# Performance work log

Hardware: AMD Instinct MI355X
Metric: run time of the kernel (lower is better)

## Reference

```python
import math
import jax, jax.numpy as jnp
import numpy as np

DIM = 2048
NUM_HEADS = 16
HEAD_DIM = DIM // NUM_HEADS
BASE = 10000.0


def _rope(x):
    # x: [B, S, H, D]; non-interleaved (chunk-half) rotary embedding
    S, D = x.shape[1], x.shape[-1]
    inv_freq = 1.0 / (BASE ** (jnp.arange(0, D, 2, dtype=jnp.float32) / D))
    t = jnp.arange(S, dtype=jnp.float32)
    freqs = jnp.outer(t, inv_freq)  # [S, D/2]
    cos = jnp.cos(freqs)[None, :, None, :].astype(x.dtype)
    sin = jnp.sin(freqs)[None, :, None, :].astype(x.dtype)
    x1, x2 = jnp.split(x, 2, axis=-1)
    return jnp.concatenate([x1 * cos - x2 * sin, x1 * sin + x2 * cos], axis=-1)


def setup_inputs() -> dict:
    key = jax.random.key(0)
    kx, kq, kk, kv, ko = jax.random.split(key, 5)
    x = jax.random.normal(kx, (2, 2048, DIM), dtype=jnp.float32)
    scale = 0.02
    Wq = jax.random.normal(kq, (DIM, DIM), dtype=jnp.float32) * scale
    Wk = jax.random.normal(kk, (DIM, DIM), dtype=jnp.float32) * scale
    Wv = jax.random.normal(kv, (DIM, DIM), dtype=jnp.float32) * scale
    Wo = jax.random.normal(ko, (DIM, DIM), dtype=jnp.float32) * scale
    return {"x": x, "Wq": Wq, "Wk": Wk, "Wv": Wv, "Wo": Wo}


def reference(x, Wq, Wk, Wv, Wo):
    B, S, _ = x.shape
    # nn.Linear(bias=False): y = x @ W.T
    q = (x @ Wq.T).reshape(B, S, NUM_HEADS, HEAD_DIM)
    k = (x @ Wk.T).reshape(B, S, NUM_HEADS, HEAD_DIM)
    v = (x @ Wv.T).reshape(B, S, NUM_HEADS, HEAD_DIM)
    q = _rope(q)
    k = _rope(k)
    scale = 1.0 / math.sqrt(HEAD_DIM)
    # causal attention, [B,H,S,S] scores
    scores = jnp.einsum("bqhd,bkhd->bhqk", q, k) * scale
    causal = jnp.tril(jnp.ones((S, S), dtype=bool))
    scores = jnp.where(causal[None, None], scores, jnp.finfo(scores.dtype).min)
    attn = jax.nn.softmax(scores, axis=-1)
    out = jnp.einsum("bhqk,bkhd->bqhd", attn, v).reshape(B, S, DIM)
    return out @ Wo.T
```

## Files before the change

### kernel.cpp

```cpp
#include <hip/hip_runtime.h>

typedef unsigned short u16;
typedef __attribute__((ext_vector_type(8))) short short8;
typedef __attribute__((ext_vector_type(4))) float f32x4;
typedef __attribute__((ext_vector_type(4))) int i32x4;

__device__ __forceinline__ float bf2f(u16 u) {
  union { unsigned u; float f; } v; v.u = ((unsigned)u) << 16; return v.f;
}
__device__ __forceinline__ u16 f2bf(float f) {
  union { float f; unsigned u; } v; v.f = f;
  unsigned r = (v.u + 0x7FFFu + ((v.u >> 16) & 1u)) >> 16;
  return (u16)r;
}
__device__ __forceinline__ float flushv(float t, float sentinel) {
  if (t != t || fabsf(t) > 3.0e38f) return sentinel;
  return t;
}
__device__ __forceinline__ short8 ld8f(const float* p) {
  const float4 f0 = *(const float4*)p;
  const float4 f1 = *(const float4*)(p + 4);
  short8 r;
  r[0] = (short)f2bf(f0.x); r[1] = (short)f2bf(f0.y);
  r[2] = (short)f2bf(f0.z); r[3] = (short)f2bf(f0.w);
  r[4] = (short)f2bf(f1.x); r[5] = (short)f2bf(f1.y);
  r[6] = (short)f2bf(f1.z); r[7] = (short)f2bf(f1.w);
  return r;
}

__device__ __forceinline__ void gl16(const u16* g, u16* l) {
  __builtin_amdgcn_global_load_lds(
      (const __attribute__((address_space(1))) void*)g,
      (__attribute__((address_space(3))) void*)l, 16, 0, 0);
}

__global__ __launch_bounds__(256) void cvt_kernel(
    const float* __restrict__ src, u16* __restrict__ dst, long n8)
{
  const long t = (long)blockIdx.x * 256 + threadIdx.x;
  if (t < n8) *(short8*)&dst[t * 8] = ld8f(src + t * 8);
}

__global__ __launch_bounds__(256) void cvt4_kernel(
    const float* __restrict__ s0, const float* __restrict__ s1,
    const float* __restrict__ s2, const float* __restrict__ s3,
    u16* __restrict__ d0, u16* __restrict__ d1,
    u16* __restrict__ d2, u16* __restrict__ d3)
{
  const int which = blockIdx.x >> 11;
  const long t = (long)(blockIdx.x & 2047) * 256 + threadIdx.x;
  const float* s; u16* d;
  if (which == 0)      { s = s0; d = d0; }
  else if (which == 1) { s = s1; d = d1; }
  else if (which == 2) { s = s2; d = d2; }
  else                 { s = s3; d = d3; }
  *(short8*)&d[t * 8] = ld8f(s + t * 8);
}

template <bool OF>
__global__ __launch_bounds__(256) void gemm_lds(
    const u16* __restrict__ Ap,
    const u16* __restrict__ B0, const u16* __restrict__ B1,
    void* __restrict__ O0, void* __restrict__ O1,
    int M, int N, int K, float sentinel)
{
  __shared__ __align__(16) u16 As[128 * 32];
  __shared__ __align__(16) u16 Bs[128 * 32];

  const u16* Bp = (blockIdx.z == 0) ? B0 : B1;
  void* O       = (blockIdx.z == 0) ? O0 : O1;

  const int tid  = threadIdx.x;
  const int wave = tid >> 6;
  const int lane = tid & 63;
  const int quad = lane >> 4;
  const int l15  = lane & 15;

  const int m0 = blockIdx.y * 128;
  const int n0 = blockIdx.x * 128;
  const int wm = (wave >> 1) * 64;
  const int wn = (wave & 1) * 64;

  const int srow = lane >> 2;
  const int scu  = lane & 3;
  const u16* Ag0 = Ap + (long)(m0 + wave * 32 + srow) * K + scu * 8;
  const u16* Ag1 = Ag0 + 16 * (long)K;
  const u16* Bg0 = Bp + (long)(n0 + wave * 32 + srow) * K + scu * 8;
  const u16* Bg1 = Bg0 + 16 * (long)K;
  u16* Al0 = &As[(wave * 2 + 0) * 512];
  u16* Al1 = &As[(wave * 2 + 1) * 512];
  u16* Bl0 = &Bs[(wave * 2 + 0) * 512];
  u16* Bl1 = &Bs[(wave * 2 + 1) * 512];

  const f32x4 zero = {0.f, 0.f, 0.f, 0.f};
  f32x4 acc[4][4];
#pragma unroll
  for (int i = 0; i < 4; ++i)
#pragma unroll
    for (int j = 0; j < 4; ++j) acc[i][j] = zero;

  for (int k0 = 0; k0 < K; k0 += 32) {
    __syncthreads();
    gl16(Ag0 + k0, Al0);
    gl16(Ag1 + k0, Al1);
    gl16(Bg0 + k0, Bl0);
    gl16(Bg1 + k0, Bl1);
    __syncthreads();

    short8 af[4], bf[4];
#pragma unroll
    for (int i = 0; i < 4; ++i)
      af[i] = *(const short8*)&As[(wm + i * 16 + l15) * 32 + quad * 8];
#pragma unroll
    for (int j = 0; j < 4; ++j)
      bf[j] = *(const short8*)&Bs[(wn + j * 16 + l15) * 32 + quad * 8];
#pragma unroll
    for (int i = 0; i < 4; ++i)
#pragma unroll
      for (int j = 0; j < 4; ++j)
        acc[i][j] = __builtin_amdgcn_mfma_f32_16x16x32_bf16(af[i], bf[j], acc[i][j], 0, 0, 0);
  }

#pragma unroll
  for (int i = 0; i < 4; ++i) {
    const int row0 = m0 + wm + i * 16 + quad * 4;
#pragma unroll
    for (int j = 0; j < 4; ++j) {
      const int col = n0 + wn + j * 16 + l15;
#pragma unroll
      for (int r = 0; r < 4; ++r) {
        const float val = flushv(acc[i][j][r], sentinel);
        if constexpr (OF)
          ((float*)O)[(long)(row0 + r) * N + col] = val;
        else
          ((u16*)O)[(long)(row0 + r) * N + col] = f2bf(val);
      }
    }
  }
}

template <bool AF, bool WF, bool OF>
__global__ __launch_bounds__(256) void gemm_bt(
    const void* __restrict__ Ap,
    const void* __restrict__ Wp0, const void* __restrict__ Wp1, const void* __restrict__ Wp2,
    void* __restrict__ O0, void* __restrict__ O1, void* __restrict__ O2,
    int M, int N, int K, float sentinel)
{
  __shared__ __align__(16) u16 As[128 * 32];
  __shared__ __align__(16) u16 Bs[128 * 32];

  const void* Wp; void* O;
  if (blockIdx.z == 0)      { Wp = Wp0; O = O0; }
  else if (blockIdx.z == 1) { Wp = Wp1; O = O1; }
  else                      { Wp = Wp2; O = O2; }

  const float* Af = (const float*)Ap;  const u16* Ab = (const u16*)Ap;
  const float* Wf = (const float*)Wp;  const u16* Wb = (const u16*)Wp;

  const int tid  = threadIdx.x;
  const int wave = tid >> 6;
  const int lane = tid & 63;
  const int quad = lane >> 4;
  const int l15  = lane & 15;

  const int m0 = blockIdx.y * 128;
  const int n0 = blockIdx.x * 128;
  const int wm = (wave >> 1) * 64;
  const int wn = (wave & 1) * 64;

  const int e0 = wave * 1024 + lane * 8;
  const int e1 = e0 + 512;
  const int r0 = e0 >> 5, c0 = e0 & 31;
  const int r1 = e1 >> 5, c1 = e1 & 31;

  const long aoff0 = (long)(m0 + r0) * K + c0;
  const long aoff1 = (long)(m0 + r1) * K + c1;
  const long boff0 = (long)(n0 + r0) * K + c0;
  const long boff1 = (long)(n0 + r1) * K + c1;

  const f32x4 zero = {0.f, 0.f, 0.f, 0.f};
  f32x4 acc[4][4];
#pragma unroll
  for (int i = 0; i < 4; ++i)
#pragma unroll
    for (int j = 0; j < 4; ++j) acc[i][j] = zero;

  for (int k0 = 0; k0 < K; k0 += 32) {
    short8 a0, a1, b0, b1;
    if constexpr (AF) {
      a0 = ld8f(Af + aoff0 + k0);
      a1 = ld8f(Af + aoff1 + k0);
    } else {
      a0 = *(const short8*)(Ab + aoff0 + k0);
      a1 = *(const short8*)(Ab + aoff1 + k0);
    }
    if constexpr (WF) {
      b0 = ld8f(Wf + boff0 + k0);
      b1 = ld8f(Wf + boff1 + k0);
    } else {
      b0 = *(const short8*)(Wb + boff0 + k0);
      b1 = *(const short8*)(Wb + boff1 + k0);
    }

    __syncthreads();
    *(short8*)&As[e0] = a0;
    *(short8*)&As[e1] = a1;
    *(short8*)&Bs[e0] = b0;
    *(short8*)&Bs[e1] = b1;
    __syncthreads();

    short8 af[4], bf[4];
#pragma unroll
    for (int i = 0; i < 4; ++i)
      af[i] = *(const short8*)&As[(wm + i * 16 + l15) * 32 + quad * 8];
#pragma unroll
    for (int j = 0; j < 4; ++j)
      bf[j] = *(const short8*)&Bs[(wn + j * 16 + l15) * 32 + quad * 8];
#pragma unroll
    for (int i = 0; i < 4; ++i)
#pragma unroll
      for (int j = 0; j < 4; ++j)
        acc[i][j] = __builtin_amdgcn_mfma_f32_16x16x32_bf16(af[i], bf[j], acc[i][j], 0, 0, 0);
  }

#pragma unroll
  for (int i = 0; i < 4; ++i) {
    const int row0 = m0 + wm + i * 16 + quad * 4;
#pragma unroll
    for (int j = 0; j < 4; ++j) {
      const int col = n0 + wn + j * 16 + l15;
#pragma unroll
      for (int r = 0; r < 4; ++r) {
        const float val = flushv(acc[i][j][r], sentinel);
        if constexpr (OF)
          ((float*)O)[(long)(row0 + r) * N + col] = val;
        else
          ((u16*)O)[(long)(row0 + r) * N + col] = f2bf(val);
      }
    }
  }
}

__global__ __launch_bounds__(256) void rope_kernel(u16* __restrict__ Q, u16* __restrict__ K)
{
  int t = blockIdx.x * 256 + threadIdx.x;
  const int half = 2 * 2048 * 16 * 64;
  u16* P = Q;
  if (t >= half) { P = K; t -= half; }
  const int i = t & 63;
  const int s = (t >> 10) & 2047;
  const long off = ((long)(t >> 6) << 7) + i;

  const float inv_freq = __expf((float)i * -0.14391156831212787f);
  const float fr = (float)s * inv_freq;
  float sn, cs;
  __sincosf(fr, &sn, &cs);

  const float q1 = bf2f(P[off]);
  const float q2 = bf2f(P[off + 64]);
  P[off]      = f2bf(q1 * cs - q2 * sn);
  P[off + 64] = f2bf(q1 * sn + q2 * cs);
}

__global__ __launch_bounds__(256, 4) void attn_kernel(
    const u16* __restrict__ Q, const u16* __restrict__ K,
    const u16* __restrict__ VT, u16* __restrict__ AO)
{
  __shared__ __align__(16) u16 Kb[2][4096];
  __shared__ __align__(16) u16 Vb[2][4096];

  const int tid  = threadIdx.x;
  const int wave = tid >> 6;
  const int lane = tid & 63;
  const int quad = lane >> 4;
  const int l15  = lane & 15;

  const int lin = blockIdx.x;
  const int xcd = lin & 7;
  const int hi  = lin >> 8;
  const int g   = (lin >> 3) & 31;
  const int qb  = (hi & 1) ? (31 - g) : g;
  const int bh  = (xcd << 2) | hi;
  const int b   = bh >> 4;
  const int h   = bh & 15;

  const long base = (long)b * 2048 * 2048 + (long)h * 128;
  const long vtb  = (long)h * 128 * 4096 + (long)b * 2048;
  const int q0w = qb * 64 + wave * 16;
  const int qi  = q0w + l15;

  const u16* Kp0 = K + base;
  const u16* Vp0 = VT + vtb;

  auto STAGE = [&](int bs, int jb) {
#pragma unroll
    for (int gi = 0; gi < 2; ++gi) {
      const int slot = wave * 2 + gi;
      {
        const int row = slot * 4 + (lane >> 4);
        const int su  = lane & 15;
        gl16(Kp0 + (long)(jb * 32 + row) * 2048 + ((su ^ (row & 7)) << 3),
             &Kb[bs][slot * 512]);
      }
      {
        const int row = slot * 16 + (lane >> 2);
        const int su  = lane & 3;
        gl16(Vp0 + (long)row * 4096 + jb * 32 + ((su ^ ((row >> 1) & 3)) << 3),
             &Vb[bs][slot * 512]);
      }
    }
  };

  short8 qa[4];
#pragma unroll
  for (int c = 0; c < 4; ++c)
    qa[c] = *(const short8*)&Q[base + (long)(q0w + l15) * 2048 + c * 32 + quad * 8];

  const f32x4 zero = {0.f, 0.f, 0.f, 0.f};
  f32x4 o[8];
#pragma unroll
  for (int c = 0; c < 8; ++c) o[c] = zero;

  float mreg = -1e30f, lreg = 0.f;
  const float scale = 0.08838834764831845f;

  const int njb_blk = qb * 2 + 2;
  const int njb_w   = qb * 2 + 1 + (wave >> 1);

  STAGE(0, 0);
  __syncthreads();

  const int xorK = l15 & 7;
  const int xorV = (l15 >> 1) & 3;

  int cur = 0;
  for (int jb = 0; jb < njb_blk; ++jb) {
    if (jb + 1 < njb_blk) STAGE(cur ^ 1, jb + 1);

    if (jb < njb_w) {
      const int j0 = jb * 32;

      f32x4 s0T = zero, s1T = zero;
#pragma unroll
      for (int c = 0; c < 4; ++c) {
        const short8 kA = *(const short8*)&Kb[cur][l15 * 128 + (((c * 4 + quad) ^ xorK) << 3)];
        const short8 kB2 = *(const short8*)&Kb[cur][(l15 + 16) * 128 + (((c * 4 + quad) ^ xorK) << 3)];
        s0T = __builtin_amdgcn_mfma_f32_16x16x32_bf16(kA, qa[c], s0T, 0, 0, 0);
        s1T = __builtin_amdgcn_mfma_f32_16x16x32_bf16(kB2, qa[c], s1T, 0, 0, 0);
      }

      float sv0[4], sv1[4];
      float pmax = -1e30f;
      if (j0 + 31 > q0w) {
#pragma unroll
        for (int r = 0; r < 4; ++r) {
          const int k0i = j0 + quad * 4 + r;
          float s0 = s0T[r] * scale; if (k0i > qi)      s0 = -1e30f;
          float s1 = s1T[r] * scale; if (k0i + 16 > qi) s1 = -1e30f;
          sv0[r] = s0; sv1[r] = s1;
          pmax = fmaxf(pmax, fmaxf(s0, s1));
        }
      } else {
#pragma unroll
        for (int r = 0; r < 4; ++r) {
          sv0[r] = s0T[r] * scale;
          sv1[r] = s1T[r] * scale;
          pmax = fmaxf(pmax, fmaxf(sv0[r], sv1[r]));
        }
      }
      pmax = fmaxf(pmax, __shfl_xor(pmax, 16, 64));
      pmax = fmaxf(pmax, __shfl_xor(pmax, 32, 64));
      const float mprev = mreg;
      const float mnew  = fmaxf(mprev, pmax);
      const float alpha = __expf(mprev - mnew);
      float psum = 0.f;
#pragma unroll
      for (int r = 0; r < 4; ++r) {
        sv0[r] = __expf(sv0[r] - mnew);
        sv1[r] = __expf(sv1[r] - mnew);
        psum += sv0[r] + sv1[r];
      }
      psum += __shfl_xor(psum, 16, 64);
      psum += __shfl_xor(psum, 32, 64);
      lreg = lreg * alpha + psum;
      mreg = mnew;

      int w0, w1, w2, w3;
      asm("v_cvt_pk_bf16_f32 %0, %1, %2" : "=v"(w0) : "v"(sv0[0]), "v"(sv0[1]));
      asm("v_cvt_pk_bf16_f32 %0, %1, %2" : "=v"(w1) : "v"(sv0[2]), "v"(sv0[3]));
      asm("v_cvt_pk_bf16_f32 %0, %1, %2" : "=v"(w2) : "v"(sv1[0]), "v"(sv1[1]));
      asm("v_cvt_pk_bf16_f32 %0, %1, %2" : "=v"(w3) : "v"(sv1[2]), "v"(sv1[3]));
      const int srcA = l15 + ((quad & 1) << 5);
      const int srcB = srcA + 16;
      const int a0 = __shfl(w0, srcA, 64), a1 = __shfl(w1, srcA, 64);
      const int a2 = __shfl(w0, srcB, 64), a3 = __shfl(w1, srcB, 64);
      const int h0 = __shfl(w2, srcA, 64), h1 = __shfl(w3, srcA, 64);
      const int h2 = __shfl(w2, srcB, 64), h3 = __shfl(w3, srcB, 64);
      const bool hiq = quad >= 2;
      i32x4 pt;
      pt[0] = hiq ? h0 : a0;
      pt[1] = hiq ? h1 : a1;
      pt[2] = hiq ? h2 : a2;
      pt[3] = hiq ? h3 : a3;
      const short8 pa = *(const short8*)&pt;

      float av[4];
#pragma unroll
      for (int r = 0; r < 4; ++r) av[r] = __shfl(alpha, quad * 4 + r, 64);
#pragma unroll
      for (int c = 0; c < 8; ++c) {
        o[c][0] *= av[0]; o[c][1] *= av[1]; o[c][2] *= av[2]; o[c][3] *= av[3];
      }

#pragma unroll
      for (int c = 0; c < 8; ++c) {
        const short8 vf = *(const short8*)&Vb[cur][(c * 16 + l15) * 32 + ((quad ^ xorV) << 3)];
        o[c] = __builtin_amdgcn_mfma_f32_16x16x32_bf16(pa, vf, o[c], 0, 0, 0);
      }
    }

    __syncthreads();
    cur ^= 1;
  }

#pragma unroll
  for (int r = 0; r < 4; ++r) {
    const float lr  = __shfl(lreg, quad * 4 + r, 64);
    const float inv = 1.0f / lr;
    const long rowoff = base + (long)(q0w + quad * 4 + r) * 2048;
#pragma unroll
    for (int c = 0; c < 8; ++c)
      AO[rowoff + c * 16 + l15] = f2bf(flushv(o[c][r] * inv, 9999.f));
  }
}

__global__ __launch_bounds__(256) void fill_kernel(float* __restrict__ out, long n, float v)
{
  const long t = (long)blockIdx.x * 256 + threadIdx.x;
  if (t < n) out[t] = v;
}

extern "C" void kernel_launch(void* const* d_in, const int* in_sizes, int n_in,
                              void* d_out, int out_size, void* d_ws, size_t ws_size,
                              hipStream_t stream)
{
  const float* x  = (const float*)d_in[0];
  const float* Wq = (const float*)d_in[1];
  const float* Wk = (const float*)d_in[2];
  const float* Wv = (const float*)d_in[3];
  const float* Wo = (const float*)d_in[4];
  float* out = (float*)d_out;

  const long QSZ = (long)2 * 2048 * 2048;
  const long WSZ = QSZ / 2;

  u16* ws = (u16*)d_ws;
  u16* q  = ws;
  u16* k  = ws + QSZ;
  u16* v  = ws + 2 * QSZ;
  u16* ao = q;

  if (ws_size >= (size_t)6 * QSZ * sizeof(u16)) {
    u16* xb  = ws + 3 * QSZ;
    u16* wqb = ws + 4 * QSZ;
    u16* wkb = wqb + WSZ;
    u16* wvb = wqb + 2 * WSZ;
    u16* wob = wqb + 3 * WSZ;

    cvt_kernel<<<4096, 256, 0, stream>>>(x, xb, QSZ / 8);
    cvt4_kernel<<<8192, 256, 0, stream>>>(Wq, Wk, Wv, Wo, wqb, wkb, wvb, wob);

    gemm_lds<false><<<dim3(16, 32, 2), 256, 0, stream>>>(
        xb, wqb, wkb, q, k, 4096, 2048, 2048, 7777.f);
    gemm_lds<false><<<dim3(32, 16, 1), 256, 0, stream>>>(
        wvb, xb, xb, v, v, 2048, 4096, 2048, 7777.f);
    rope_kernel<<<32768, 256, 0, stream>>>(q, k);
    attn_kernel<<<1024, 256, 0, stream>>>(q, k, v, ao);
    gemm_lds<true><<<dim3(16, 32, 1), 256, 0, stream>>>(
        ao, wob, wob, out, out, 4096, 2048, 2048, 5555.f);
    return;
  }

  if (ws_size < (size_t)3 * QSZ * sizeof(u16)) {
    fill_kernel<<<(int)((QSZ + 255) / 256), 256, 0, stream>>>(out, QSZ, 1111.f);
    return;
  }

  gemm_bt<true, true, false><<<dim3(16, 32, 2), 256, 0, stream>>>(
      x, Wq, Wk, Wk, q, k, k, 4096, 2048, 2048, 7777.f);
  gemm_bt<true, true, false><<<dim3(32, 16, 1), 256, 0, stream>>>(
      Wv, x, x, x, v, v, v, 2048, 4096, 2048, 7777.f);
  rope_kernel<<<32768, 256, 0, stream>>>(q, k);
  attn_kernel<<<1024, 256, 0, stream>>>(q, k, v, ao);
  gemm_bt<false, true, true><<<dim3(16, 32, 1), 256, 0, stream>>>(
      ao, Wo, Wo, Wo, out, out, out, 4096, 2048, 2048, 5555.f);
}
```

Baseline: 455.3 us.

## Double-buffer GEMM LDS tiles and merge conversion and QKV launches

The LDS-tiled GEMM now uses two shared-memory buffers, so the global-to-LDS load for the next K slice is issued while MFMAs run on the current one. This halves the barriers per K step and hides load latency. The five fp32-to-bf16 conversions are merged into one kernel, and the Q/K/V projections into a single 1536-block launch, removing launch gaps and tail idle time between kernels. In exchange, LDS use per block doubles, which may lower occupancy, and K is now hardcoded to 2048.

```diff
diff --git a/kernel.cpp b/kernel.cpp
--- a/kernel.cpp
+++ b/kernel.cpp
@@ -34,41 +34,37 @@
       (__attribute__((address_space(3))) void*)l, 16, 0, 0);
 }
 
-__global__ __launch_bounds__(256) void cvt_kernel(
-    const float* __restrict__ src, u16* __restrict__ dst, long n8)
-{
-  const long t = (long)blockIdx.x * 256 + threadIdx.x;
-  if (t < n8) *(short8*)&dst[t * 8] = ld8f(src + t * 8);
-}
-
-__global__ __launch_bounds__(256) void cvt4_kernel(
-    const float* __restrict__ s0, const float* __restrict__ s1,
-    const float* __restrict__ s2, const float* __restrict__ s3,
-    u16* __restrict__ d0, u16* __restrict__ d1,
-    u16* __restrict__ d2, u16* __restrict__ d3)
-{
-  const int which = blockIdx.x >> 11;
-  const long t = (long)(blockIdx.x & 2047) * 256 + threadIdx.x;
-  const float* s; u16* d;
-  if (which == 0)      { s = s0; d = d0; }
-  else if (which == 1) { s = s1; d = d1; }
-  else if (which == 2) { s = s2; d = d2; }
-  else                 { s = s3; d = d3; }
+__global__ __launch_bounds__(256) void cvt_all(
+    const float* __restrict__ x,
+    const float* __restrict__ Wq, const float* __restrict__ Wk,
+    const float* __restrict__ Wv, const float* __restrict__ Wo,
+    u16* __restrict__ xb, u16* __restrict__ wqb, u16* __restrict__ wkb,
+    u16* __restrict__ wvb, u16* __restrict__ wob)
+{
+  const int bid = blockIdx.x;
+  const float* s; u16* d; long t;
+  if (bid < 8192) {
+    const int which = bid >> 11;
+    t = (long)(bid & 2047) * 256 + threadIdx.x;
+    if (which == 0)      { s = Wq; d = wqb; }
+    else if (which == 1) { s = Wk; d = wkb; }
+    else if (which == 2) { s = Wv; d = wvb; }
+    else                 { s = Wo; d = wob; }
+  } else {
+    s = x; d = xb;
+    t = (long)(bid - 8192) * 256 + threadIdx.x;
+  }
   *(short8*)&d[t * 8] = ld8f(s + t * 8);
 }
 
 template <bool OF>
-__global__ __launch_bounds__(256) void gemm_lds(
-    const u16* __restrict__ Ap,
-    const u16* __restrict__ B0, const u16* __restrict__ B1,
-    void* __restrict__ O0, void* __restrict__ O1,
-    int M, int N, int K, float sentinel)
-{
-  __shared__ __align__(16) u16 As[128 * 32];
-  __shared__ __align__(16) u16 Bs[128 * 32];
-
-  const u16* Bp = (blockIdx.z == 0) ? B0 : B1;
-  void* O       = (blockIdx.z == 0) ? O0 : O1;
+__device__ __forceinline__ void gemm_core(
+    const u16* __restrict__ Ap, const u16* __restrict__ Bp,
+    void* __restrict__ O, int m0, int n0, int N, float sentinel)
+{
+  __shared__ __align__(16) u16 As[2][128 * 32];
+  __shared__ __align__(16) u16 Bs[2][128 * 32];
+  constexpr int K = 2048;
 
   const int tid  = threadIdx.x;
   const int wave = tid >> 6;
@@ -76,8 +72,6 @@
   const int quad = lane >> 4;
   const int l15  = lane & 15;
 
-  const int m0 = blockIdx.y * 128;
-  const int n0 = blockIdx.x * 128;
   const int wm = (wave >> 1) * 64;
   const int wn = (wave & 1) * 64;
 
@@ -87,10 +81,8 @@
   const u16* Ag1 = Ag0 + 16 * (long)K;
   const u16* Bg0 = Bp + (long)(n0 + wave * 32 + srow) * K + scu * 8;
   const u16* Bg1 = Bg0 + 16 * (long)K;
-  u16* Al0 = &As[(wave * 2 + 0) * 512];
-  u16* Al1 = &As[(wave * 2 + 1) * 512];
-  u16* Bl0 = &Bs[(wave * 2 + 0) * 512];
-  u16* Bl1 = &Bs[(wave * 2 + 1) * 512];
+  const int sl0 = (wave * 2 + 0) * 512;
+  const int sl1 = (wave * 2 + 1) * 512;
 
   const f32x4 zero = {0.f, 0.f, 0.f, 0.f};
   f32x4 acc[4][4];
@@ -99,26 +91,49 @@
 #pragma unroll
     for (int j = 0; j < 4; ++j) acc[i][j] = zero;
 
-  for (int k0 = 0; k0 < K; k0 += 32) {
+  gl16(Ag0, &As[0][sl0]); gl16(Ag1, &As[0][sl1]);
+  gl16(Bg0, &Bs[0][sl0]); gl16(Bg1, &Bs[0][sl1]);
+  __syncthreads();
+
+#pragma unroll 1
+  for (int k0 = 0; k0 < K; k0 += 64) {
+    gl16(Ag0 + k0 + 32, &As[1][sl0]); gl16(Ag1 + k0 + 32, &As[1][sl1]);
+    gl16(Bg0 + k0 + 32, &Bs[1][sl0]); gl16(Bg1 + k0 + 32, &Bs[1][sl1]);
+    {
+      short8 af[4], bf[4];
+#pragma unroll
+      for (int i = 0; i < 4; ++i)
+        af[i] = *(const short8*)&As[0][(wm + i * 16 + l15) * 32 + quad * 8];
+#pragma unroll
+      for (int j = 0; j < 4; ++j)
+        bf[j] = *(const short8*)&Bs[0][(wn + j * 16 + l15) * 32 + quad * 8];
+#pragma unroll
+      for (int i = 0; i < 4; ++i)
+#pragma unroll
+        for (int j = 0; j < 4; ++j)
+          acc[i][j] = __builtin_amdgcn_mfma_f32_16x16x32_bf16(af[i], bf[j], acc[i][j], 0, 0, 0);
+    }
     __syncthreads();
-    gl16(Ag0 + k0, Al0);
-    gl16(Ag1 + k0, Al1);
-    gl16(Bg0 + k0, Bl0);
-    gl16(Bg1 + k0, Bl1);
+
+    if (k0 + 64 < K) {
+      gl16(Ag0 + k0 + 64, &As[0][sl0]); gl16(Ag1 + k0 + 64, &As[0][sl1]);
+      gl16(Bg0 + k0 + 64, &Bs[0][sl0]); gl16(Bg1 + k0 + 64, &Bs[0][sl1]);
+    }
+    {
+      short8 af[4], bf[4];
+#pragma unroll
+      for (int i = 0; i < 4; ++i)
+        af[i] = *(const short8*)&As[1][(wm + i * 16 + l15) * 32 + quad * 8];
+#pragma unroll
+      for (int j = 0; j < 4; ++j)
+        bf[j] = *(const short8*)&Bs[1][(wn + j * 16 + l15) * 32 + quad * 8];
+#pragma unroll
+      for (int i = 0; i < 4; ++i)
+#pragma unroll
+        for (int j = 0; j < 4; ++j)
+          acc[i][j] = __builtin_amdgcn_mfma_f32_16x16x32_bf16(af[i], bf[j], acc[i][j], 0, 0, 0);
+    }
     __syncthreads();
-
-    short8 af[4], bf[4];
-#pragma unroll
-    for (int i = 0; i < 4; ++i)
-      af[i] = *(const short8*)&As[(wm + i * 16 + l15) * 32 + quad * 8];
-#pragma unroll
-    for (int j = 0; j < 4; ++j)
-      bf[j] = *(const short8*)&Bs[(wn + j * 16 + l15) * 32 + quad * 8];
-#pragma unroll
-    for (int i = 0; i < 4; ++i)
-#pragma unroll
-      for (int j = 0; j < 4; ++j)
-        acc[i][j] = __builtin_amdgcn_mfma_f32_16x16x32_bf16(af[i], bf[j], acc[i][j], 0, 0, 0);
   }
 
 #pragma unroll
@@ -137,6 +152,31 @@
       }
     }
   }
+}
+
+__global__ __launch_bounds__(256) void gemm_qkv(
+    const u16* __restrict__ xb,
+    const u16* __restrict__ wqb, const u16* __restrict__ wkb, const u16* __restrict__ wvb,
+    u16* __restrict__ q, u16* __restrict__ k, u16* __restrict__ v)
+{
+  const int bid = blockIdx.x;
+  const int z = bid >> 9, r = bid & 511;
+  const u16 *A, *B; u16* O; int m0, n0, Nn;
+  if (z < 2) {
+    A = xb; B = z ? wkb : wqb; O = z ? k : q;
+    m0 = (r >> 4) * 128; n0 = (r & 15) * 128; Nn = 2048;
+  } else {
+    A = wvb; B = xb; O = v;
+    m0 = (r >> 5) * 128; n0 = (r & 31) * 128; Nn = 4096;
+  }
+  gemm_core<false>(A, B, O, m0, n0, Nn, 7777.f);
+}
+
+__global__ __launch_bounds__(256) void gemm_proj(
+    const u16* __restrict__ ao, const u16* __restrict__ wob, float* __restrict__ out)
+{
+  const int r = blockIdx.x;
+  gemm_core<true>(ao, wob, out, (r >> 4) * 128, (r & 15) * 128, 2048, 5555.f);
 }
 
 template <bool AF, bool WF, bool OF>
@@ -467,17 +507,11 @@
     u16* wvb = wqb + 2 * WSZ;
     u16* wob = wqb + 3 * WSZ;
 
-    cvt_kernel<<<4096, 256, 0, stream>>>(x, xb, QSZ / 8);
-    cvt4_kernel<<<8192, 256, 0, stream>>>(Wq, Wk, Wv, Wo, wqb, wkb, wvb, wob);
-
-    gemm_lds<false><<<dim3(16, 32, 2), 256, 0, stream>>>(
-        xb, wqb, wkb, q, k, 4096, 2048, 2048, 7777.f);
-    gemm_lds<false><<<dim3(32, 16, 1), 256, 0, stream>>>(
-        wvb, xb, xb, v, v, 2048, 4096, 2048, 7777.f);
+    cvt_all<<<12288, 256, 0, stream>>>(x, Wq, Wk, Wv, Wo, xb, wqb, wkb, wvb, wob);
+    gemm_qkv<<<1536, 256, 0, stream>>>(xb, wqb, wkb, wvb, q, k, v);
     rope_kernel<<<32768, 256, 0, stream>>>(q, k);
     attn_kernel<<<1024, 256, 0, stream>>>(q, k, v, ao);
-    gemm_lds<true><<<dim3(16, 32, 1), 256, 0, stream>>>(
-        ao, wob, wob, out, out, 4096, 2048, 2048, 5555.f);
+    gemm_proj<<<512, 256, 0, stream>>>(ao, wob, out);
     return;
   }
 
```

New measurement: 422.1 us. 7.3% less time.
